# Optimization experiments

Hardware: AMD Instinct MI355X
Metric: run time of the kernel (lower is better)

The kernel has to match this reference:

```python
import jax, jax.numpy as jnp
import numpy as np

H = 64  # hidden_dim


def _lstm_layer(x, w_ih, w_hh, b_ih, b_hh):
    # x: [B,T,I]; w_ih: [4H,I]; w_hh: [4H,H]; gate order (PyTorch): i,f,g,o
    B = x.shape[0]
    xp = jnp.einsum('bti,gi->btg', x, w_ih) + b_ih + b_hh  # [B,T,4H]
    h0 = jnp.zeros((B, H), x.dtype)
    c0 = jnp.zeros((B, H), x.dtype)

    def step(carry, xt):
        h, c = carry
        g = xt + h @ w_hh.T  # [B,4H]
        i, f, gg, o = jnp.split(g, 4, axis=-1)
        c = jax.nn.sigmoid(f) * c + jax.nn.sigmoid(i) * jnp.tanh(gg)
        h = jax.nn.sigmoid(o) * jnp.tanh(c)
        return (h, c), h

    _, ys = jax.lax.scan(step, (h0, c0), xp.transpose(1, 0, 2))  # [T,B,H]
    return ys.transpose(1, 0, 2)


def _gru_layer(x, w_ih, w_hh, b_ih, b_hh):
    # x: [B,T,I]; w_ih: [3H,I]; w_hh: [3H,H]; gate order (PyTorch): r,z,n
    B = x.shape[0]
    xp = jnp.einsum('bti,gi->btg', x, w_ih) + b_ih  # [B,T,3H]
    h0 = jnp.zeros((B, H), x.dtype)

    def step(h, xt):
        hp = h @ w_hh.T + b_hh  # [B,3H]
        xr, xz, xn = jnp.split(xt, 3, axis=-1)
        hr, hz, hn = jnp.split(hp, 3, axis=-1)
        r = jax.nn.sigmoid(xr + hr)
        z = jax.nn.sigmoid(xz + hz)
        n = jnp.tanh(xn + r * hn)
        h = (1.0 - z) * n + z * h
        return h, h

    _, ys = jax.lax.scan(step, h0, xp.transpose(1, 0, 2))
    return ys.transpose(1, 0, 2)


def setup_inputs() -> dict:
    key = jax.random.key(0)
    ks = jax.random.split(key, 20)
    s = 1.0 / np.sqrt(H)  # PyTorch default uniform(-1/sqrt(H), 1/sqrt(H))
    u = lambda k, shp: jax.random.uniform(k, shp, jnp.float32, -s, s)
    B, T, I = 2048, 512, 1
    return {
        'x': jax.random.normal(ks[0], (B, T, I), jnp.float32),
        # LSTM layer 0 (input I) and layer 1 (input H)
        'lw_ih0': u(ks[1], (4 * H, I)), 'lw_hh0': u(ks[2], (4 * H, H)),
        'lb_ih0': u(ks[3], (4 * H,)), 'lb_hh0': u(ks[4], (4 * H,)),
        'lw_ih1': u(ks[5], (4 * H, H)), 'lw_hh1': u(ks[6], (4 * H, H)),
        'lb_ih1': u(ks[7], (4 * H,)), 'lb_hh1': u(ks[8], (4 * H,)),
        # GRU layer 0 and 1 (input H)
        'gw_ih0': u(ks[9], (3 * H, H)), 'gw_hh0': u(ks[10], (3 * H, H)),
        'gb_ih0': u(ks[11], (3 * H,)), 'gb_hh0': u(ks[12], (3 * H,)),
        'gw_ih1': u(ks[13], (3 * H, H)), 'gw_hh1': u(ks[14], (3 * H, H)),
        'gb_ih1': u(ks[15], (3 * H,)), 'gb_hh1': u(ks[16], (3 * H,)),
        # fc head
        'fc_w': u(ks[17], (1, H)), 'fc_b': u(ks[18], (1,)),
    }


def reference(x, lw_ih0, lw_hh0, lb_ih0, lb_hh0, lw_ih1, lw_hh1, lb_ih1, lb_hh1,
              gw_ih0, gw_hh0, gb_ih0, gb_hh0, gw_ih1, gw_hh1, gb_ih1, gb_hh1,
              fc_w, fc_b):
    out = _lstm_layer(x, lw_ih0, lw_hh0, lb_ih0, lb_hh0)
    out = _lstm_layer(out, lw_ih1, lw_hh1, lb_ih1, lb_hh1)
    out = _gru_layer(out, gw_ih0, gw_hh0, gb_ih0, gb_hh0)
    out = _gru_layer(out, gw_ih1, gw_hh1, gb_ih1, gb_hh1)
    return out[:, -1, :] @ fc_w.T + fc_b  # [B,1]
```

## Files before the change

kernel.cpp:

```cpp
#include <hip/hip_runtime.h>


#define TT 512
#define SR 72
#define XR 68
#define LOG2E 1.44269504f

typedef __attribute__((ext_vector_type(8))) short bfrag;
typedef __attribute__((ext_vector_type(4))) float facc;

#define MFMA(a,b,c) __builtin_amdgcn_mfma_f32_16x16x32_bf16((a),(b),(c),0,0,0)

__device__ __forceinline__ short f2bf(float f){
  union { float f; unsigned u; } v; v.f = f;
  return (short)((v.u + 0x7fffu + ((v.u >> 16) & 1u)) >> 16);
}
__device__ __forceinline__ float sigmP(float u){
  return __builtin_amdgcn_rcpf(1.0f + __builtin_amdgcn_exp2f(u));
}
__device__ __forceinline__ float tanhP(float u){
  return 2.0f * __builtin_amdgcn_rcpf(1.0f + __builtin_amdgcn_exp2f(u)) - 1.0f;
}

__global__ __launch_bounds__(1024, 4) void rnn_fused(
    const float* __restrict__ x,
    const float* __restrict__ lw_ih0, const float* __restrict__ lw_hh0,
    const float* __restrict__ lb_ih0, const float* __restrict__ lb_hh0,
    const float* __restrict__ lw_ih1, const float* __restrict__ lw_hh1,
    const float* __restrict__ lb_ih1, const float* __restrict__ lb_hh1,
    const float* __restrict__ gw_ih0, const float* __restrict__ gw_hh0,
    const float* __restrict__ gb_ih0, const float* __restrict__ gb_hh0,
    const float* __restrict__ gw_ih1, const float* __restrict__ gw_hh1,
    const float* __restrict__ gb_ih1, const float* __restrict__ gb_hh1,
    const float* __restrict__ fc_w, const float* __restrict__ fc_b,
    float* __restrict__ out)
{
  __shared__ __align__(16) short S0[2][16 * SR];
  __shared__ __align__(16) short S1[2][16 * SR];
  __shared__ __align__(16) short S2[2][16 * SR];
  __shared__ __align__(16) short S3[2][16 * SR];
  __shared__ float xs[8][XR];
  __shared__ float hfin[8][XR];

  const int tid = threadIdx.x;
  const int w     = tid >> 6;
  const int layer = w >> 2;
  const int lo4   = w & 3;
  const int l   = tid & 63;
  const int lq  = l >> 4;
  const int lc  = l & 15;
  const int kb  = lq * 8;
  const int rb0 = blockIdx.x * 8;
  const int wrbase = (4 * lq) * SR + lo4 * 16 + lc;

  const float SS  = -LOG2E;
  const float ST2 = -2.0f * LOG2E;

  for (int i = tid; i < 16 * SR; i += 1024) {
    S0[0][i] = 0; S0[1][i] = 0; S1[0][i] = 0; S1[1][i] = 0;
    S2[0][i] = 0; S2[1][i] = 0; S3[0][i] = 0; S3[1][i] = 0;
  }
  __syncthreads();

  #define STAGE_X()                                                    \
    if ((T & 63) == 0 && T < TT) {                                     \
      if (tid < 512) xs[tid >> 6][tid & 63] =                          \
          x[(rb0 + (tid >> 6)) * TT + T + (tid & 63)];                 \
      __syncthreads();                                                 \
    }

  if (layer == 0) {
    bfrag wf[4][2];
    float wxs[4], bs[4];
    #pragma unroll
    for (int G = 0; G < 4; ++G) {
      const float sc = (G == 2) ? ST2 : SS;
      const int col = G * 64 + lo4 * 16 + lc;
      #pragma unroll
      for (int kt = 0; kt < 2; ++kt) {
        bfrag f;
        #pragma unroll
        for (int j = 0; j < 8; ++j)
          f[j] = f2bf(sc * lw_hh0[col * 64 + kt * 32 + kb + j]);
        wf[G][kt] = f;
      }
      wxs[G] = sc * lw_ih0[col];
      bs[G]  = sc * (lb_ih0[col] + lb_hh0[col]);
    }
    float c0[2] = {0, 0};
    #pragma unroll 2
    for (int T = 0; T < TT + 3; ++T) {
      const int cur = T & 1, prv = cur ^ 1;
      STAGE_X();
      if (T < TT) {
        const short* s = S0[prv];
        const bfrag a0 = *(const bfrag*)(s + lc * SR + kb);
        const bfrag a1 = *(const bfrag*)(s + lc * SR + 32 + kb);
        facc acc[4];
        #pragma unroll
        for (int G = 0; G < 4; ++G) {
          facc z = {0,0,0,0};
          z = MFMA(a0, wf[G][0], z);
          z = MFMA(a1, wf[G][1], z);
          acc[G] = z;
        }
        #pragma unroll
        for (int m = 0; m < 2; ++m) {
          const float xv = xs[2 * lq + m][T & 63];
          const float i_ = sigmP(acc[0][m] + xv * wxs[0] + bs[0]);
          const float f_ = sigmP(acc[1][m] + xv * wxs[1] + bs[1]);
          const float g_ = tanhP(acc[2][m] + xv * wxs[2] + bs[2]);
          const float o_ = sigmP(acc[3][m] + xv * wxs[3] + bs[3]);
          c0[m] = f_ * c0[m] + i_ * g_;
          S0[cur][wrbase + m * SR] = f2bf(o_ * tanhP(c0[m] * ST2));
        }
      }
      __syncthreads();
    }
  } else if (layer == 1) {
    bfrag wxf[4][2], whf[4][2];
    float bs[4];
    #pragma unroll
    for (int G = 0; G < 4; ++G) {
      const float sc = (G == 2) ? ST2 : SS;
      const int col = G * 64 + lo4 * 16 + lc;
      #pragma unroll
      for (int kt = 0; kt < 2; ++kt) {
        bfrag f0, f1;
        #pragma unroll
        for (int j = 0; j < 8; ++j) {
          const int o = col * 64 + kt * 32 + kb + j;
          f0[j] = f2bf(sc * lw_ih1[o]);
          f1[j] = f2bf(sc * lw_hh1[o]);
        }
        wxf[G][kt] = f0; whf[G][kt] = f1;
      }
      bs[G] = sc * (lb_ih1[col] + lb_hh1[col]);
    }
    float c1[2] = {0, 0};
    #pragma unroll 2
    for (int T = 0; T < TT + 3; ++T) {
      const int cur = T & 1, prv = cur ^ 1;
      STAGE_X();
      if (T >= 1 && T <= TT) {
        const short* sx = S0[prv];
        const short* sh = S1[prv];
        const bfrag ax0 = *(const bfrag*)(sx + lc * SR + kb);
        const bfrag ax1 = *(const bfrag*)(sx + lc * SR + 32 + kb);
        const bfrag ah0 = *(const bfrag*)(sh + lc * SR + kb);
        const bfrag ah1 = *(const bfrag*)(sh + lc * SR + 32 + kb);
        facc acc[4];
        #pragma unroll
        for (int G = 0; G < 4; ++G) {
          facc z = {0,0,0,0};
          z = MFMA(ax0, wxf[G][0], z);
          z = MFMA(ax1, wxf[G][1], z);
          facc y = {0,0,0,0};
          y = MFMA(ah0, whf[G][0], y);
          y = MFMA(ah1, whf[G][1], y);
          #pragma unroll
          for (int m = 0; m < 4; ++m) z[m] += y[m];
          acc[G] = z;
        }
        #pragma unroll
        for (int m = 0; m < 2; ++m) {
          const float i_ = sigmP(acc[0][m] + bs[0]);
          const float f_ = sigmP(acc[1][m] + bs[1]);
          const float g_ = tanhP(acc[2][m] + bs[2]);
          const float o_ = sigmP(acc[3][m] + bs[3]);
          c1[m] = f_ * c1[m] + i_ * g_;
          S1[cur][wrbase + m * SR] = f2bf(o_ * tanhP(c1[m] * ST2));
        }
      }
      __syncthreads();
    }
  } else if (layer == 2) {
    bfrag gxf[3][2], ghf[3][2];
    float brz[2], bnx, bnh;
    #pragma unroll
    for (int G = 0; G < 3; ++G) {
      const float sc = (G == 2) ? ST2 : SS;
      const int col = G * 64 + lo4 * 16 + lc;
      #pragma unroll
      for (int kt = 0; kt < 2; ++kt) {
        bfrag f0, f1;
        #pragma unroll
        for (int j = 0; j < 8; ++j) {
          const int o = col * 64 + kt * 32 + kb + j;
          f0[j] = f2bf(sc * gw_ih0[o]);
          f1[j] = f2bf(sc * gw_hh0[o]);
        }
        gxf[G][kt] = f0; ghf[G][kt] = f1;
      }
      if (G < 2) brz[G] = sc * (gb_ih0[col] + gb_hh0[col]);
      else { bnx = sc * gb_ih0[col]; bnh = sc * gb_hh0[col]; }
    }
    float h2[2] = {0, 0};
    #pragma unroll 2
    for (int T = 0; T < TT + 3; ++T) {
      const int cur = T & 1, prv = cur ^ 1;
      STAGE_X();
      if (T >= 2 && T <= TT + 1) {
        const short* sx = S1[prv];
        const short* sh = S2[prv];
        const bfrag ax0 = *(const bfrag*)(sx + lc * SR + kb);
        const bfrag ax1 = *(const bfrag*)(sx + lc * SR + 32 + kb);
        const bfrag ah0 = *(const bfrag*)(sh + lc * SR + kb);
        const bfrag ah1 = *(const bfrag*)(sh + lc * SR + 32 + kb);
        facc ax[3], ah[3];
        #pragma unroll
        for (int G = 0; G < 3; ++G) {
          facc z = {0,0,0,0};
          z = MFMA(ax0, gxf[G][0], z);
          z = MFMA(ax1, gxf[G][1], z);
          ax[G] = z;
          facc y = {0,0,0,0};
          y = MFMA(ah0, ghf[G][0], y);
          y = MFMA(ah1, ghf[G][1], y);
          ah[G] = y;
        }
        #pragma unroll
        for (int m = 0; m < 2; ++m) {
          const float r_ = sigmP(ax[0][m] + ah[0][m] + brz[0]);
          const float z_ = sigmP(ax[1][m] + ah[1][m] + brz[1]);
          const float n_ = tanhP((ax[2][m] + bnx) + r_ * (ah[2][m] + bnh));
          h2[m] = n_ + z_ * (h2[m] - n_);
          S2[cur][wrbase + m * SR] = f2bf(h2[m]);
        }
      }
      __syncthreads();
    }
  } else {
    bfrag gxf[3][2], ghf[3][2];
    float brz[2], bnx, bnh;
    #pragma unroll
    for (int G = 0; G < 3; ++G) {
      const float sc = (G == 2) ? ST2 : SS;
      const int col = G * 64 + lo4 * 16 + lc;
      #pragma unroll
      for (int kt = 0; kt < 2; ++kt) {
        bfrag f0, f1;
        #pragma unroll
        for (int j = 0; j < 8; ++j) {
          const int o = col * 64 + kt * 32 + kb + j;
          f0[j] = f2bf(sc * gw_ih1[o]);
          f1[j] = f2bf(sc * gw_hh1[o]);
        }
        gxf[G][kt] = f0; ghf[G][kt] = f1;
      }
      if (G < 2) brz[G] = sc * (gb_ih1[col] + gb_hh1[col]);
      else { bnx = sc * gb_ih1[col]; bnh = sc * gb_hh1[col]; }
    }
    float h3[2] = {0, 0};
    #pragma unroll 2
    for (int T = 0; T < TT + 3; ++T) {
      const int cur = T & 1, prv = cur ^ 1;
      STAGE_X();
      if (T >= 3) {
        const short* sx = S2[prv];
        const short* sh = S3[prv];
        const bfrag ax0 = *(const bfrag*)(sx + lc * SR + kb);
        const bfrag ax1 = *(const bfrag*)(sx + lc * SR + 32 + kb);
        const bfrag ah0 = *(const bfrag*)(sh + lc * SR + kb);
        const bfrag ah1 = *(const bfrag*)(sh + lc * SR + 32 + kb);
        facc ax[3], ah[3];
        #pragma unroll
        for (int G = 0; G < 3; ++G) {
          facc z = {0,0,0,0};
          z = MFMA(ax0, gxf[G][0], z);
          z = MFMA(ax1, gxf[G][1], z);
          ax[G] = z;
          facc y = {0,0,0,0};
          y = MFMA(ah0, ghf[G][0], y);
          y = MFMA(ah1, ghf[G][1], y);
          ah[G] = y;
        }
        #pragma unroll
        for (int m = 0; m < 2; ++m) {
          const float r_ = sigmP(ax[0][m] + ah[0][m] + brz[0]);
          const float z_ = sigmP(ax[1][m] + ah[1][m] + brz[1]);
          const float n_ = tanhP((ax[2][m] + bnx) + r_ * (ah[2][m] + bnh));
          h3[m] = n_ + z_ * (h3[m] - n_);
          S3[cur][wrbase + m * SR] = f2bf(h3[m]);
        }
      }
      __syncthreads();
    }
    #pragma unroll
    for (int m = 0; m < 2; ++m)
      hfin[2 * lq + m][lo4 * 16 + lc] = h3[m];
  }

  __syncthreads();
  if (tid < 8) {
    float s = fc_b[0];
    #pragma unroll 8
    for (int d = 0; d < 64; ++d) s += hfin[tid][d] * fc_w[d];
    out[rb0 + tid] = s;
  }
}

extern "C" void kernel_launch(void* const* d_in, const int* in_sizes, int n_in,
                              void* d_out, int out_size, void* d_ws, size_t ws_size,
                              hipStream_t stream) {
  const float* x      = (const float*)d_in[0];
  const float* lw_ih0 = (const float*)d_in[1];
  const float* lw_hh0 = (const float*)d_in[2];
  const float* lb_ih0 = (const float*)d_in[3];
  const float* lb_hh0 = (const float*)d_in[4];
  const float* lw_ih1 = (const float*)d_in[5];
  const float* lw_hh1 = (const float*)d_in[6];
  const float* lb_ih1 = (const float*)d_in[7];
  const float* lb_hh1 = (const float*)d_in[8];
  const float* gw_ih0 = (const float*)d_in[9];
  const float* gw_hh0 = (const float*)d_in[10];
  const float* gb_ih0 = (const float*)d_in[11];
  const float* gb_hh0 = (const float*)d_in[12];
  const float* gw_ih1 = (const float*)d_in[13];
  const float* gw_hh1 = (const float*)d_in[14];
  const float* gb_ih1 = (const float*)d_in[15];
  const float* gb_hh1 = (const float*)d_in[16];
  const float* fc_w   = (const float*)d_in[17];
  const float* fc_b   = (const float*)d_in[18];

  rnn_fused<<<dim3(2048 / 8), dim3(1024), 0, stream>>>(
      x, lw_ih0, lw_hh0, lb_ih0, lb_hh0, lw_ih1, lw_hh1, lb_ih1, lb_hh1,
      gw_ih0, gw_hh0, gb_ih0, gb_hh0, gw_ih1, gw_hh1, gb_ih1, gb_hh1,
      fc_w, fc_b, (float*)d_out);
}
```

Baseline: 423.8 us.

## Halve rows per block and widen per-wave columns to use more CUs

Each block now handles 4 batch rows with 512 threads (2 waves per layer) instead of 8 rows with 1024 threads, so the grid doubles to 512 blocks. Each wave computes 32 hidden columns (two 16-column MFMA tiles per gate), and LSTM and GRU r/z accumulations are chained into a single MFMA accumulator. The whole x sequence for the block's rows is preloaded into shared memory once, which removes the periodic staging barriers. The cost is more weight registers per wave and the 16-row MFMA tiles now carry only 4 useful rows, so more MFMA work is wasted per useful row.

```diff
diff --git a/kernel.cpp b/kernel.cpp
--- a/kernel.cpp
+++ b/kernel.cpp
@@ -3,7 +3,6 @@
 
 #define TT 512
 #define SR 72
-#define XR 68
 #define LOG2E 1.44269504f
 
 typedef __attribute__((ext_vector_type(8))) short bfrag;
@@ -22,7 +21,7 @@
   return 2.0f * __builtin_amdgcn_rcpf(1.0f + __builtin_amdgcn_exp2f(u)) - 1.0f;
 }
 
-__global__ __launch_bounds__(1024, 4) void rnn_fused(
+__global__ __launch_bounds__(512) void rnn_fused(
     const float* __restrict__ x,
     const float* __restrict__ lw_ih0, const float* __restrict__ lw_hh0,
     const float* __restrict__ lb_ih0, const float* __restrict__ lb_hh0,
@@ -39,109 +38,113 @@
   __shared__ __align__(16) short S1[2][16 * SR];
   __shared__ __align__(16) short S2[2][16 * SR];
   __shared__ __align__(16) short S3[2][16 * SR];
-  __shared__ float xs[8][XR];
-  __shared__ float hfin[8][XR];
+  __shared__ float xs[4][TT];
+  __shared__ float hfin[4][68];
 
   const int tid = threadIdx.x;
   const int w     = tid >> 6;
-  const int layer = w >> 2;
-  const int lo4   = w & 3;
+  const int layer = w >> 1;
+  const int lo2   = w & 1;
   const int l   = tid & 63;
   const int lq  = l >> 4;
   const int lc  = l & 15;
   const int kb  = lq * 8;
-  const int rb0 = blockIdx.x * 8;
-  const int wrbase = (4 * lq) * SR + lo4 * 16 + lc;
+  const int rb0 = blockIdx.x * 4;
+  const int wrb = (4 * lq) * SR + lo2 * 32 + lc;
 
   const float SS  = -LOG2E;
   const float ST2 = -2.0f * LOG2E;
 
-  for (int i = tid; i < 16 * SR; i += 1024) {
+  {
+    const int idx = tid * 4;
+    const int row = idx >> 9, t = idx & 511;
+    *(float4*)&xs[row][t] = *(const float4*)(x + (rb0 + row) * TT + t);
+  }
+  for (int i = tid; i < 16 * SR; i += 512) {
     S0[0][i] = 0; S0[1][i] = 0; S1[0][i] = 0; S1[1][i] = 0;
     S2[0][i] = 0; S2[1][i] = 0; S3[0][i] = 0; S3[1][i] = 0;
   }
   __syncthreads();
 
-  #define STAGE_X()                                                    \
-    if ((T & 63) == 0 && T < TT) {                                     \
-      if (tid < 512) xs[tid >> 6][tid & 63] =                          \
-          x[(rb0 + (tid >> 6)) * TT + T + (tid & 63)];                 \
-      __syncthreads();                                                 \
-    }
-
   if (layer == 0) {
-    bfrag wf[4][2];
-    float wxs[4], bs[4];
+    bfrag wf[4][2][2];
+    float wxs[4][2], bs[4][2];
     #pragma unroll
     for (int G = 0; G < 4; ++G) {
       const float sc = (G == 2) ? ST2 : SS;
-      const int col = G * 64 + lo4 * 16 + lc;
       #pragma unroll
-      for (int kt = 0; kt < 2; ++kt) {
-        bfrag f;
-        #pragma unroll
-        for (int j = 0; j < 8; ++j)
-          f[j] = f2bf(sc * lw_hh0[col * 64 + kt * 32 + kb + j]);
-        wf[G][kt] = f;
-      }
-      wxs[G] = sc * lw_ih0[col];
-      bs[G]  = sc * (lb_ih0[col] + lb_hh0[col]);
-    }
-    float c0[2] = {0, 0};
+      for (int ct = 0; ct < 2; ++ct) {
+        const int col = G * 64 + lo2 * 32 + ct * 16 + lc;
+        #pragma unroll
+        for (int kt = 0; kt < 2; ++kt) {
+          bfrag f;
+          #pragma unroll
+          for (int j = 0; j < 8; ++j)
+            f[j] = f2bf(sc * lw_hh0[col * 64 + kt * 32 + kb + j]);
+          wf[G][ct][kt] = f;
+        }
+        wxs[G][ct] = sc * lw_ih0[col];
+        bs[G][ct]  = sc * (lb_ih0[col] + lb_hh0[col]);
+      }
+    }
+    float c0[2] = {0.f, 0.f};
     #pragma unroll 2
     for (int T = 0; T < TT + 3; ++T) {
       const int cur = T & 1, prv = cur ^ 1;
-      STAGE_X();
       if (T < TT) {
         const short* s = S0[prv];
         const bfrag a0 = *(const bfrag*)(s + lc * SR + kb);
         const bfrag a1 = *(const bfrag*)(s + lc * SR + 32 + kb);
-        facc acc[4];
-        #pragma unroll
-        for (int G = 0; G < 4; ++G) {
-          facc z = {0,0,0,0};
-          z = MFMA(a0, wf[G][0], z);
-          z = MFMA(a1, wf[G][1], z);
-          acc[G] = z;
-        }
-        #pragma unroll
-        for (int m = 0; m < 2; ++m) {
-          const float xv = xs[2 * lq + m][T & 63];
-          const float i_ = sigmP(acc[0][m] + xv * wxs[0] + bs[0]);
-          const float f_ = sigmP(acc[1][m] + xv * wxs[1] + bs[1]);
-          const float g_ = tanhP(acc[2][m] + xv * wxs[2] + bs[2]);
-          const float o_ = sigmP(acc[3][m] + xv * wxs[3] + bs[3]);
-          c0[m] = f_ * c0[m] + i_ * g_;
-          S0[cur][wrbase + m * SR] = f2bf(o_ * tanhP(c0[m] * ST2));
+        facc acc[4][2];
+        #pragma unroll
+        for (int G = 0; G < 4; ++G)
+          #pragma unroll
+          for (int ct = 0; ct < 2; ++ct) {
+            facc z = {0,0,0,0};
+            z = MFMA(a0, wf[G][ct][0], z);
+            z = MFMA(a1, wf[G][ct][1], z);
+            acc[G][ct] = z;
+          }
+        const float xv = xs[lq][T];
+        #pragma unroll
+        for (int ct = 0; ct < 2; ++ct) {
+          const float i_ = sigmP(acc[0][ct][0] + xv * wxs[0][ct] + bs[0][ct]);
+          const float f_ = sigmP(acc[1][ct][0] + xv * wxs[1][ct] + bs[1][ct]);
+          const float g_ = tanhP(acc[2][ct][0] + xv * wxs[2][ct] + bs[2][ct]);
+          const float o_ = sigmP(acc[3][ct][0] + xv * wxs[3][ct] + bs[3][ct]);
+          c0[ct] = f_ * c0[ct] + i_ * g_;
+          S0[cur][wrb + ct * 16] = f2bf(o_ * tanhP(c0[ct] * ST2));
         }
       }
       __syncthreads();
     }
   } else if (layer == 1) {
-    bfrag wxf[4][2], whf[4][2];
-    float bs[4];
+    bfrag wxf[4][2][2], whf[4][2][2];
+    float bs[4][2];
     #pragma unroll
     for (int G = 0; G < 4; ++G) {
       const float sc = (G == 2) ? ST2 : SS;
-      const int col = G * 64 + lo4 * 16 + lc;
       #pragma unroll
-      for (int kt = 0; kt < 2; ++kt) {
-        bfrag f0, f1;
-        #pragma unroll
-        for (int j = 0; j < 8; ++j) {
-          const int o = col * 64 + kt * 32 + kb + j;
-          f0[j] = f2bf(sc * lw_ih1[o]);
-          f1[j] = f2bf(sc * lw_hh1[o]);
-        }
-        wxf[G][kt] = f0; whf[G][kt] = f1;
-      }
-      bs[G] = sc * (lb_ih1[col] + lb_hh1[col]);
-    }
-    float c1[2] = {0, 0};
+      for (int ct = 0; ct < 2; ++ct) {
+        const int col = G * 64 + lo2 * 32 + ct * 16 + lc;
+        #pragma unroll
+        for (int kt = 0; kt < 2; ++kt) {
+          bfrag f0, f1;
+          #pragma unroll
+          for (int j = 0; j < 8; ++j) {
+            const int o = col * 64 + kt * 32 + kb + j;
+            f0[j] = f2bf(sc * lw_ih1[o]);
+            f1[j] = f2bf(sc * lw_hh1[o]);
+          }
+          wxf[G][ct][kt] = f0; whf[G][ct][kt] = f1;
+        }
+        bs[G][ct] = sc * (lb_ih1[col] + lb_hh1[col]);
+      }
+    }
+    float c1[2] = {0.f, 0.f};
     #pragma unroll 2
     for (int T = 0; T < TT + 3; ++T) {
       const int cur = T & 1, prv = cur ^ 1;
-      STAGE_X();
       if (T >= 1 && T <= TT) {
         const short* sx = S0[prv];
         const short* sh = S1[prv];
@@ -149,57 +152,58 @@
         const bfrag ax1 = *(const bfrag*)(sx + lc * SR + 32 + kb);
         const bfrag ah0 = *(const bfrag*)(sh + lc * SR + kb);
         const bfrag ah1 = *(const bfrag*)(sh + lc * SR + 32 + kb);
-        facc acc[4];
-        #pragma unroll
-        for (int G = 0; G < 4; ++G) {
-          facc z = {0,0,0,0};
-          z = MFMA(ax0, wxf[G][0], z);
-          z = MFMA(ax1, wxf[G][1], z);
-          facc y = {0,0,0,0};
-          y = MFMA(ah0, whf[G][0], y);
-          y = MFMA(ah1, whf[G][1], y);
-          #pragma unroll
-          for (int m = 0; m < 4; ++m) z[m] += y[m];
-          acc[G] = z;
-        }
-        #pragma unroll
-        for (int m = 0; m < 2; ++m) {
-          const float i_ = sigmP(acc[0][m] + bs[0]);
-          const float f_ = sigmP(acc[1][m] + bs[1]);
-          const float g_ = tanhP(acc[2][m] + bs[2]);
-          const float o_ = sigmP(acc[3][m] + bs[3]);
-          c1[m] = f_ * c1[m] + i_ * g_;
-          S1[cur][wrbase + m * SR] = f2bf(o_ * tanhP(c1[m] * ST2));
+        facc acc[4][2];
+        #pragma unroll
+        for (int G = 0; G < 4; ++G)
+          #pragma unroll
+          for (int ct = 0; ct < 2; ++ct) {
+            facc z = {0,0,0,0};
+            z = MFMA(ax0, wxf[G][ct][0], z);
+            z = MFMA(ax1, wxf[G][ct][1], z);
+            z = MFMA(ah0, whf[G][ct][0], z);
+            z = MFMA(ah1, whf[G][ct][1], z);
+            acc[G][ct] = z;
+          }
+        #pragma unroll
+        for (int ct = 0; ct < 2; ++ct) {
+          const float i_ = sigmP(acc[0][ct][0] + bs[0][ct]);
+          const float f_ = sigmP(acc[1][ct][0] + bs[1][ct]);
+          const float g_ = tanhP(acc[2][ct][0] + bs[2][ct]);
+          const float o_ = sigmP(acc[3][ct][0] + bs[3][ct]);
+          c1[ct] = f_ * c1[ct] + i_ * g_;
+          S1[cur][wrb + ct * 16] = f2bf(o_ * tanhP(c1[ct] * ST2));
         }
       }
       __syncthreads();
     }
   } else if (layer == 2) {
-    bfrag gxf[3][2], ghf[3][2];
-    float brz[2], bnx, bnh;
+    bfrag gxf[3][2][2], ghf[3][2][2];
+    float brz[2][2], bnx[2], bnh[2];
     #pragma unroll
     for (int G = 0; G < 3; ++G) {
       const float sc = (G == 2) ? ST2 : SS;
-      const int col = G * 64 + lo4 * 16 + lc;
       #pragma unroll
-      for (int kt = 0; kt < 2; ++kt) {
-        bfrag f0, f1;
-        #pragma unroll
-        for (int j = 0; j < 8; ++j) {
-          const int o = col * 64 + kt * 32 + kb + j;
-          f0[j] = f2bf(sc * gw_ih0[o]);
-          f1[j] = f2bf(sc * gw_hh0[o]);
-        }
-        gxf[G][kt] = f0; ghf[G][kt] = f1;
-      }
-      if (G < 2) brz[G] = sc * (gb_ih0[col] + gb_hh0[col]);
-      else { bnx = sc * gb_ih0[col]; bnh = sc * gb_hh0[col]; }
-    }
-    float h2[2] = {0, 0};
+      for (int ct = 0; ct < 2; ++ct) {
+        const int col = G * 64 + lo2 * 32 + ct * 16 + lc;
+        #pragma unroll
+        for (int kt = 0; kt < 2; ++kt) {
+          bfrag f0, f1;
+          #pragma unroll
+          for (int j = 0; j < 8; ++j) {
+            const int o = col * 64 + kt * 32 + kb + j;
+            f0[j] = f2bf(sc * gw_ih0[o]);
+            f1[j] = f2bf(sc * gw_hh0[o]);
+          }
+          gxf[G][ct][kt] = f0; ghf[G][ct][kt] = f1;
+        }
+        if (G < 2) brz[G][ct] = sc * (gb_ih0[col] + gb_hh0[col]);
+        else { bnx[ct] = sc * gb_ih0[col]; bnh[ct] = sc * gb_hh0[col]; }
+      }
+    }
+    float h2[2] = {0.f, 0.f};
     #pragma unroll 2
     for (int T = 0; T < TT + 3; ++T) {
       const int cur = T & 1, prv = cur ^ 1;
-      STAGE_X();
       if (T >= 2 && T <= TT + 1) {
         const short* sx = S1[prv];
         const short* sh = S2[prv];
@@ -207,55 +211,64 @@
         const bfrag ax1 = *(const bfrag*)(sx + lc * SR + 32 + kb);
         const bfrag ah0 = *(const bfrag*)(sh + lc * SR + kb);
         const bfrag ah1 = *(const bfrag*)(sh + lc * SR + 32 + kb);
-        facc ax[3], ah[3];
-        #pragma unroll
-        for (int G = 0; G < 3; ++G) {
-          facc z = {0,0,0,0};
-          z = MFMA(ax0, gxf[G][0], z);
-          z = MFMA(ax1, gxf[G][1], z);
-          ax[G] = z;
-          facc y = {0,0,0,0};
-          y = MFMA(ah0, ghf[G][0], y);
-          y = MFMA(ah1, ghf[G][1], y);
-          ah[G] = y;
-        }
-        #pragma unroll
-        for (int m = 0; m < 2; ++m) {
-          const float r_ = sigmP(ax[0][m] + ah[0][m] + brz[0]);
-          const float z_ = sigmP(ax[1][m] + ah[1][m] + brz[1]);
-          const float n_ = tanhP((ax[2][m] + bnx) + r_ * (ah[2][m] + bnh));
-          h2[m] = n_ + z_ * (h2[m] - n_);
-          S2[cur][wrbase + m * SR] = f2bf(h2[m]);
+        facc rz[2][2], axn[2], ahn[2];
+        #pragma unroll
+        for (int ct = 0; ct < 2; ++ct) {
+          #pragma unroll
+          for (int G = 0; G < 2; ++G) {
+            facc z = {0,0,0,0};
+            z = MFMA(ax0, gxf[G][ct][0], z);
+            z = MFMA(ax1, gxf[G][ct][1], z);
+            z = MFMA(ah0, ghf[G][ct][0], z);
+            z = MFMA(ah1, ghf[G][ct][1], z);
+            rz[G][ct] = z;
+          }
+          facc a_ = {0,0,0,0}, b_ = {0,0,0,0};
+          a_ = MFMA(ax0, gxf[2][ct][0], a_);
+          a_ = MFMA(ax1, gxf[2][ct][1], a_);
+          b_ = MFMA(ah0, ghf[2][ct][0], b_);
+          b_ = MFMA(ah1, ghf[2][ct][1], b_);
+          axn[ct] = a_; ahn[ct] = b_;
+        }
+        #pragma unroll
+        for (int ct = 0; ct < 2; ++ct) {
+          const float r_ = sigmP(rz[0][ct][0] + brz[0][ct]);
+          const float z_ = sigmP(rz[1][ct][0] + brz[1][ct]);
+          const float n_ = tanhP((axn[ct][0] + bnx[ct]) + r_ * (ahn[ct][0] + bnh[ct]));
+          h2[ct] = n_ + z_ * (h2[ct] - n_);
+          S2[cur][wrb + ct * 16] = f2bf(h2[ct]);
         }
       }
       __syncthreads();
     }
   } else {
-    bfrag gxf[3][2], ghf[3][2];
-    float brz[2], bnx, bnh;
+    bfrag gxf[3][2][2], ghf[3][2][2];
+    float brz[2][2], bnx[2], bnh[2];
     #pragma unroll
     for (int G = 0; G < 3; ++G) {
       const float sc = (G == 2) ? ST2 : SS;
-      const int col = G * 64 + lo4 * 16 + lc;
       #pragma unroll
-      for (int kt = 0; kt < 2; ++kt) {
-        bfrag f0, f1;
-        #pragma unroll
-        for (int j = 0; j < 8; ++j) {
-          const int o = col * 64 + kt * 32 + kb + j;
-          f0[j] = f2bf(sc * gw_ih1[o]);
-          f1[j] = f2bf(sc * gw_hh1[o]);
-        }
-        gxf[G][kt] = f0; ghf[G][kt] = f1;
-      }
-      if (G < 2) brz[G] = sc * (gb_ih1[col] + gb_hh1[col]);
-      else { bnx = sc * gb_ih1[col]; bnh = sc * gb_hh1[col]; }
-    }
-    float h3[2] = {0, 0};
+      for (int ct = 0; ct < 2; ++ct) {
+        const int col = G * 64 + lo2 * 32 + ct * 16 + lc;
+        #pragma unroll
+        for (int kt = 0; kt < 2; ++kt) {
+          bfrag f0, f1;
+          #pragma unroll
+          for (int j = 0; j < 8; ++j) {
+            const int o = col * 64 + kt * 32 + kb + j;
+            f0[j] = f2bf(sc * gw_ih1[o]);
+            f1[j] = f2bf(sc * gw_hh1[o]);
+          }
+          gxf[G][ct][kt] = f0; ghf[G][ct][kt] = f1;
+        }
+        if (G < 2) brz[G][ct] = sc * (gb_ih1[col] + gb_hh1[col]);
+        else { bnx[ct] = sc * gb_ih1[col]; bnh[ct] = sc * gb_hh1[col]; }
+      }
+    }
+    float h3[2] = {0.f, 0.f};
     #pragma unroll 2
     for (int T = 0; T < TT + 3; ++T) {
       const int cur = T & 1, prv = cur ^ 1;
-      STAGE_X();
       if (T >= 3) {
         const short* sx = S2[prv];
         const short* sh = S3[prv];
@@ -263,36 +276,42 @@
         const bfrag ax1 = *(const bfrag*)(sx + lc * SR + 32 + kb);
         const bfrag ah0 = *(const bfrag*)(sh + lc * SR + kb);
         const bfrag ah1 = *(const bfrag*)(sh + lc * SR + 32 + kb);
-        facc ax[3], ah[3];
-        #pragma unroll
-        for (int G = 0; G < 3; ++G) {
-          facc z = {0,0,0,0};
-          z = MFMA(ax0, gxf[G][0], z);
-          z = MFMA(ax1, gxf[G][1], z);
-          ax[G] = z;
-          facc y = {0,0,0,0};
-          y = MFMA(ah0, ghf[G][0], y);
-          y = MFMA(ah1, ghf[G][1], y);
-          ah[G] = y;
-        }
-        #pragma unroll
-        for (int m = 0; m < 2; ++m) {
-          const float r_ = sigmP(ax[0][m] + ah[0][m] + brz[0]);
-          const float z_ = sigmP(ax[1][m] + ah[1][m] + brz[1]);
-          const float n_ = tanhP((ax[2][m] + bnx) + r_ * (ah[2][m] + bnh));
-          h3[m] = n_ + z_ * (h3[m] - n_);
-          S3[cur][wrbase + m * SR] = f2bf(h3[m]);
+        facc rz[2][2], axn[2], ahn[2];
+        #pragma unroll
+        for (int ct = 0; ct < 2; ++ct) {
+          #pragma unroll
+          for (int G = 0; G < 2; ++G) {
+            facc z = {0,0,0,0};
+            z = MFMA(ax0, gxf[G][ct][0], z);
+            z = MFMA(ax1, gxf[G][ct][1], z);
+            z = MFMA(ah0, ghf[G][ct][0], z);
+            z = MFMA(ah1, ghf[G][ct][1], z);
+            rz[G][ct] = z;
+          }
+          facc a_ = {0,0,0,0}, b_ = {0,0,0,0};
+          a_ = MFMA(ax0, gxf[2][ct][0], a_);
+          a_ = MFMA(ax1, gxf[2][ct][1], a_);
+          b_ = MFMA(ah0, ghf[2][ct][0], b_);
+          b_ = MFMA(ah1, ghf[2][ct][1], b_);
+          axn[ct] = a_; ahn[ct] = b_;
+        }
+        #pragma unroll
+        for (int ct = 0; ct < 2; ++ct) {
+          const float r_ = sigmP(rz[0][ct][0] + brz[0][ct]);
+          const float z_ = sigmP(rz[1][ct][0] + brz[1][ct]);
+          const float n_ = tanhP((axn[ct][0] + bnx[ct]) + r_ * (ahn[ct][0] + bnh[ct]));
+          h3[ct] = n_ + z_ * (h3[ct] - n_);
+          S3[cur][wrb + ct * 16] = f2bf(h3[ct]);
         }
       }
       __syncthreads();
     }
-    #pragma unroll
-    for (int m = 0; m < 2; ++m)
-      hfin[2 * lq + m][lo4 * 16 + lc] = h3[m];
+    hfin[lq][lo2 * 32 + lc]      = h3[0];
+    hfin[lq][lo2 * 32 + 16 + lc] = h3[1];
   }
 
   __syncthreads();
-  if (tid < 8) {
+  if (tid < 4) {
     float s = fc_b[0];
     #pragma unroll 8
     for (int d = 0; d < 64; ++d) s += hfin[tid][d] * fc_w[d];
@@ -323,7 +342,7 @@
   const float* fc_w   = (const float*)d_in[17];
   const float* fc_b   = (const float*)d_in[18];
 
-  rnn_fused<<<dim3(2048 / 8), dim3(1024), 0, stream>>>(
+  rnn_fused<<<dim3(2048 / 4), dim3(512), 0, stream>>>(
       x, lw_ih0, lw_hh0, lb_ih0, lb_hh0, lw_ih1, lw_hh1, lb_ih1, lb_hh1,
       gw_ih0, gw_hh0, gb_ih0, gb_hh0, gw_ih1, gw_hh1, gb_ih1, gb_hh1,
       fc_w, fc_b, (float*)d_out);
```

Result: slower. 681.4 us (+60.8%).
